# Kernel optimization log

Measured on AMD Instinct MI355X. Metric: run time of the kernel, lower is better.

## Reference

```python
import jax, jax.numpy as jnp
import numpy as np
import math

B, S, H, NH = 2, 1024, 768, 12
DH = H // NH  # 64

def setup_inputs() -> dict:
    key = jax.random.key(0)
    ks = jax.random.split(key, 8)
    sc = 0.02
    return {
        "hidden_states": jax.random.normal(ks[0], (B, S, H), jnp.float32),
        "bbox_pos_emb": jax.random.normal(ks[1], (S, S, B, DH), jnp.float32),
        "attention_mask": jnp.zeros((B, 1, 1, S), jnp.float32),
        "Wq": jax.random.normal(ks[2], (H, H), jnp.float32) * sc,
        "bq": jnp.zeros((H,), jnp.float32),
        "Wk": jax.random.normal(ks[3], (H, H), jnp.float32) * sc,
        "bk": jnp.zeros((H,), jnp.float32),
        "Wv": jax.random.normal(ks[4], (H, H), jnp.float32) * sc,
        "bv": jnp.zeros((H,), jnp.float32),
    }

def reference(hidden_states, bbox_pos_emb, attention_mask, Wq, bq, Wk, bk, Wv, bv):
    b, s, h = hidden_states.shape
    def proj(W, bias):
        # (b, s, h) -> (b, nh, s, dh)
        y = hidden_states @ W.T + bias
        return y.reshape(b, s, NH, DH).transpose(0, 2, 1, 3)
    q = proj(Wq, bq)
    k = proj(Wk, bk)
    v = proj(Wv, bv)
    # QK^T: (b, nh, s, s)
    scores = jnp.einsum("bnid,bnjd->bnij", q, k)
    # bbox bias: (s, s, b, dh) -> (b, s, s, dh); bnid,bijd->bnij
    bbox = bbox_pos_emb.transpose(2, 0, 1, 3)
    scores = scores + jnp.einsum("bnid,bijd->bnij", q, bbox)
    scores = scores / math.sqrt(DH)
    scores = scores + attention_mask
    probs = jax.nn.softmax(scores, axis=-1)
    ctx = jnp.einsum("bnij,bnjd->bnid", probs, v)
    ctx = ctx.transpose(0, 2, 1, 3).reshape(b, s, h)
    return ctx
```

## Files before the change

kernel.cpp:

```cpp
#include <hip/hip_runtime.h>
#include <hip/hip_bf16.h>

typedef short bf4 __attribute__((ext_vector_type(4)));
typedef short short8 __attribute__((ext_vector_type(8)));
typedef float f32x4 __attribute__((ext_vector_type(4)));

#define MFMA(a, b, c) __builtin_amdgcn_mfma_f32_16x16x32_bf16((a), (b), (c), 0, 0, 0)

#define NB 2
#define NS 1024
#define NHID 768
#define NHEAD 12
#define NDH 64

__device__ __forceinline__ short f2bf(float x) {
    __hip_bfloat16 h = __float2bfloat16(x);
    return *reinterpret_cast<short*>(&h);
}

__device__ __forceinline__ int xcd_swz(int orig, int nwg) {
    return (orig & 7) * (nwg >> 3) + (orig >> 3);
}

typedef const __attribute__((address_space(1))) void gas_t;
typedef __attribute__((address_space(3))) void las_t;
__device__ __forceinline__ void gld_lds16(const float* g, float* l) {
    __builtin_amdgcn_global_load_lds((gas_t*)g, (las_t*)l, 16, 0, 0);
}
__device__ __forceinline__ void gld_lds16s(const short* g, short* l) {
    __builtin_amdgcn_global_load_lds((gas_t*)g, (las_t*)l, 16, 0, 0);
}

#define NHE (2048 * 768)
#define WE  (768 * 768)
__global__ void cvt_bf16_all(
    const float* __restrict__ hidden,
    const float* __restrict__ Wq, const float* __restrict__ Wk,
    const float* __restrict__ Wv,
    short* __restrict__ Xbf, short* __restrict__ Wbf)
{
    const int base = (blockIdx.x * 256 + threadIdx.x) * 4;
    const float* src; short* dst; int off;
    if (base < NHE)               { src = hidden; dst = Xbf;          off = base; }
    else if (base < NHE + WE)     { src = Wq;     dst = Wbf;          off = base - NHE; }
    else if (base < NHE + 2 * WE) { src = Wk;     dst = Wbf + WE;     off = base - NHE - WE; }
    else                          { src = Wv;     dst = Wbf + 2 * WE; off = base - NHE - 2 * WE; }
    f32x4 v = *reinterpret_cast<const f32x4*>(src + off);
    bf4 r;
    r[0] = f2bf(v[0]); r[1] = f2bf(v[1]); r[2] = f2bf(v[2]); r[3] = f2bf(v[3]);
    *reinterpret_cast<bf4*>(dst + off) = r;
}

__device__ __forceinline__ void qkv_block(
    int m0, int n0,
    const short* __restrict__ Xbf, const short* __restrict__ Wbf,
    const float* __restrict__ bq, const float* __restrict__ bk,
    const float* __restrict__ bv,
    short* __restrict__ Qo, short* __restrict__ Ko, short* __restrict__ VTo,
    short (*Alds)[4096], short (*Blds)[4096])
{
    const int lane = threadIdx.x & 63;
    const int wave = threadIdx.x >> 6;
    const int lg = lane >> 4, lr = lane & 15;

    const int proj = n0 / NHID;
    const int ncol0 = n0 % NHID;
    const float* bias = proj == 0 ? bq : (proj == 1 ? bk : bv);

    f32x4 acc[4];
    #pragma unroll
    for (int s = 0; s < 4; ++s) acc[s] = (f32x4){0.f, 0.f, 0.f, 0.f};

    auto stage = [&](int t, int buf) {
        const int k0 = t * 64;
        #pragma unroll
        for (int p = 0; p < 2; ++p) {
            const int op = wave * 2 + p;
            const int unit = op * 64 + lane;
            const int r = unit >> 3, u = unit & 7;
            const int g = u ^ (r & 7);
            gld_lds16s(Xbf + (size_t)(m0 + r) * NHID + k0 + g * 8,
                       &Alds[buf][op * 512]);
        }
        #pragma unroll
        for (int p = 0; p < 2; ++p) {
            const int op = wave * 2 + p;
            const int unit = op * 64 + lane;
            const int r = unit >> 3, u = unit & 7;
            const int g = u ^ (r & 7);
            gld_lds16s(Wbf + (size_t)(n0 + r) * NHID + k0 + g * 8,
                       &Blds[buf][op * 512]);
        }
    };

    auto compute = [&](int buf) {
        #pragma unroll
        for (int kk = 0; kk < 2; ++kk) {
            const int U = kk * 4 + lg;
            const int Ra = wave * 16 + lr;
            short8 a = *reinterpret_cast<const short8*>(
                &Alds[buf][(Ra * 8 + (U ^ (Ra & 7))) * 8]);
            #pragma unroll
            for (int s = 0; s < 4; ++s) {
                const int R = s * 16 + lr;
                short8 b = *reinterpret_cast<const short8*>(
                    &Blds[buf][(R * 8 + (U ^ (R & 7))) * 8]);
                acc[s] = MFMA(a, b, acc[s]);
            }
        }
    };

    stage(0, 0);
    for (int t = 0; t < 12; ++t) {
        if (t < 11) {
            stage(t + 1, (t + 1) % 3);
            asm volatile("s_waitcnt vmcnt(4)" ::: "memory");
        } else {
            asm volatile("s_waitcnt vmcnt(0)" ::: "memory");
        }
        __builtin_amdgcn_s_barrier();
        compute(t % 3);
    }

    #pragma unroll
    for (int s = 0; s < 4; ++s) {
        const int ncol = ncol0 + s * 16 + lr;
        const float badd = bias[ncol];
        #pragma unroll
        for (int r = 0; r < 4; ++r) {
            const int m = m0 + wave * 16 + lg * 4 + r;
            const short v16 = f2bf(acc[s][r] + badd);
            if (proj == 0) {
                Qo[(size_t)m * NHID + ncol] = v16;
            } else if (proj == 1) {
                Ko[(size_t)m * NHID + ncol] = v16;
            } else {
                const int b = m >> 10, ss = m & 1023;
                const int h = ncol >> 6, dd = ncol & 63;
                VTo[(((size_t)(b * NHEAD + h) * NDH + dd) << 10) + ss] = v16;
            }
        }
    }
}

__device__ __forceinline__ void bias_block(
    int i,
    const short* __restrict__ Q,
    const float* __restrict__ bbox,
    const float* __restrict__ mask,
    short* __restrict__ biasH,
    float (*lds)[2][2048])
{
    const int lane = threadIdx.x & 63;
    const int wave = threadIdx.x >> 6;
    const int lg = lane >> 4, lr = lane & 15;
    const int jq = wave * 256;

    short8 qa[2][2];
    #pragma unroll
    for (int b2 = 0; b2 < 2; ++b2)
        #pragma unroll
        for (int kk = 0; kk < 2; ++kk)
            qa[b2][kk] = *reinterpret_cast<const short8*>(
                Q + ((size_t)(b2 * NS) + i) * NHID + lr * 64 + kk * 32 + lg * 8);

    const int r_half = lane >> 5;
    const int u_lin = lane & 31;

    auto stage = [&](int t, int buf) {
        const int j0 = jq + t * 16;
        float* dst = &lds[wave][buf][0];
        #pragma unroll
        for (int w = 0; w < 8; ++w) {
            const int r = 2 * w + r_half;
            const int u = u_lin ^ (r & 7);
            const float* src = bbox + (size_t)(i * NS + j0 + r) * 128 + u * 4;
            gld_lds16(src, dst + w * 256);
        }
    };

    auto compute = [&](int t, int buf) {
        const float* tile = &lds[wave][buf][0];
        const int j0 = jq + t * 16;
        const int x = lr & 7;
        #pragma unroll
        for (int b2 = 0; b2 < 2; ++b2) {
            const float mk = mask[b2 * NS + j0 + lr];
            f32x4 c = (f32x4){0.f, 0.f, 0.f, 0.f};
            #pragma unroll
            for (int kk = 0; kk < 2; ++kk) {
                const int q0 = b2 * 16 + kk * 8 + lg * 2;
                f32x4 ca = *reinterpret_cast<const f32x4*>(tile + (size_t)(lr * 32 + ((q0)     ^ x)) * 4);
                f32x4 cb = *reinterpret_cast<const f32x4*>(tile + (size_t)(lr * 32 + ((q0 + 1) ^ x)) * 4);
                short8 bf;
                bf[0] = f2bf(ca[0]); bf[1] = f2bf(ca[1]); bf[2] = f2bf(ca[2]); bf[3] = f2bf(ca[3]);
                bf[4] = f2bf(cb[0]); bf[5] = f2bf(cb[1]); bf[6] = f2bf(cb[2]); bf[7] = f2bf(cb[3]);
                c = MFMA(qa[b2][kk], bf, c);
            }
            if (lg < 3) {
                #pragma unroll
                for (int r = 0; r < 4; ++r) {
                    const int n = lg * 4 + r;
                    biasH[((size_t)(b2 * NHEAD + n) * NS + i) * NS + j0 + lr] =
                        f2bf(c[r] * 0.125f + mk);
                }
            }
        }
    };

    stage(0, 0);
    for (int t = 0; t < 16; ++t) {
        const int buf = t & 1;
        asm volatile("s_waitcnt lgkmcnt(0)" ::: "memory");
        if (t < 15) stage(t + 1, buf ^ 1);
        if (t == 0 || t == 15) asm volatile("s_waitcnt vmcnt(8)"  ::: "memory");
        else                   asm volatile("s_waitcnt vmcnt(16)" ::: "memory");
        compute(t, buf);
    }
}

__global__ __launch_bounds__(256, 3) void q_gemm(
    const short* __restrict__ Xbf, const short* __restrict__ Wbf,
    const float* __restrict__ bq, const float* __restrict__ bk,
    const float* __restrict__ bv,
    short* __restrict__ Qo, short* __restrict__ Ko, short* __restrict__ VTo)
{
    __shared__ short Alds[3][4096];
    __shared__ short Blds[3][4096];
    const int s = xcd_swz(blockIdx.x, 384);
    const int m0 = (s / 12) * 64;
    const int n0 = (s % 12) * 64;
    qkv_block(m0, n0, Xbf, Wbf, bq, bk, bv, Qo, Ko, VTo, Alds, Blds);
}

__global__ __launch_bounds__(256, 2) void bias_kv(
    const short* __restrict__ Qw,
    const float* __restrict__ bbox,
    const float* __restrict__ mask,
    short* __restrict__ biasH,
    const short* __restrict__ Xbf, const short* __restrict__ Wbf,
    const float* __restrict__ bq, const float* __restrict__ bk,
    const float* __restrict__ bv,
    short* __restrict__ Ko, short* __restrict__ VTo)
{
    __shared__ __align__(16) char smem[65536];
    const int bid = blockIdx.x;
    const int grp = bid / 7, rem = bid % 7;
    if (rem < 4) {
        const int i = grp * 4 + rem;
        bias_block(i, Qw, bbox, mask, biasH, (float(*)[2][2048])smem);
    } else {
        const int kvid = grp * 3 + (rem - 4);
        const int s = xcd_swz(kvid, 768);
        const int m0 = (s / 24) * 64;
        const int n0 = NHID + (s % 24) * 64;
        qkv_block(m0, n0, Xbf, Wbf, bq, bk, bv,
                  nullptr, Ko, VTo,
                  (short(*)[4096])smem, (short(*)[4096])(smem + 24576));
    }
}

__global__ __launch_bounds__(256, 3) void attn3(
    const short* __restrict__ Q,
    const short* __restrict__ K,
    const short* __restrict__ VT,
    const short* __restrict__ biasH,
    float* __restrict__ out)
{
    const int tid = threadIdx.x;
    const int lane = tid & 63;
    const int wave = tid >> 6;
    const int lg = lane >> 4, lr = lane & 15;

    const int wgid = xcd_swz(blockIdx.x, 24 * 16);
    const int bh = wgid >> 4;
    const int ic = wgid & 15;
    const int b = bh / NHEAD, h = bh % NHEAD;
    const int i0 = ic * 64 + wave * 16;

    __shared__ short Klds[3][2048];
    __shared__ short Vlds[3][2048];
    __shared__ short Blds[3][2048];
    __shared__ short plds[4][16 * 40];

    short8 qa[2];
    #pragma unroll
    for (int kk = 0; kk < 2; ++kk)
        qa[kk] = *reinterpret_cast<const short8*>(
            Q + ((size_t)(b * NS) + i0 + lr) * NHID + h * 64 + kk * 32 + lg * 8);

    const short* Kb = K + (size_t)b * NS * NHID + h * 64;
    const short* Vb = VT + (size_t)(b * NHEAD + h) * NDH * NS;
    const short* Bb = biasH + ((size_t)(b * NHEAD + h) * NS + ic * 64) * NS;

    f32x4 ctx[4];
    #pragma unroll
    for (int dt = 0; dt < 4; ++dt) ctx[dt] = (f32x4){0.f, 0.f, 0.f, 0.f};
    f32x4 den = (f32x4){0.f, 0.f, 0.f, 0.f};

    const int kr = tid >> 3, ku = tid & 7;
    const int kgu = ku ^ (kr & 7);
    const int vr = tid >> 2, vu = tid & 3;
    const int vgu = vu ^ (vr & 3);
    const int br = tid >> 2, bu = tid & 3;

    auto stage = [&](int t, int buf) {
        const int j0 = t * 32;
        gld_lds16s(Kb + (size_t)(j0 + kr) * NHID + kgu * 8, &Klds[buf][tid * 8]);
        gld_lds16s(Vb + (size_t)vr * NS + j0 + vgu * 8,     &Vlds[buf][tid * 8]);
        gld_lds16s(Bb + (size_t)br * NS + j0 + bu * 8,      &Blds[buf][tid * 8]);
    };

    auto compute = [&](int buf) {
        f32x4 sc[2];
        #pragma unroll
        for (int s = 0; s < 2; ++s) {
            f32x4 c = (f32x4){0.f, 0.f, 0.f, 0.f};
            #pragma unroll
            for (int kk = 0; kk < 2; ++kk) {
                const int R = s * 16 + lr;
                const int U = kk * 4 + lg;
                short8 kf = *reinterpret_cast<const short8*>(
                    &Klds[buf][(R * 8 + (U ^ (R & 7))) * 8]);
                c = MFMA(qa[kk], kf, c);
            }
            sc[s] = c;
        }
        #pragma unroll
        for (int s = 0; s < 2; ++s)
            #pragma unroll
            for (int r = 0; r < 4; ++r) {
                const unsigned int u = (unsigned int)(unsigned short)
                    Blds[buf][wave * 512 + (lg * 4 + r) * 32 + s * 16 + lr] << 16;
                float bb;
                __builtin_memcpy(&bb, &u, 4);
                sc[s][r] = __expf(sc[s][r] * 0.125f + bb);
            }
        den += sc[0] + sc[1];

        #pragma unroll
        for (int s = 0; s < 2; ++s)
            #pragma unroll
            for (int r = 0; r < 4; ++r)
                plds[wave][(lg * 4 + r) * 40 + s * 16 + lr] = f2bf(sc[s][r]);
        asm volatile("" ::: "memory");
        short8 pa = *reinterpret_cast<const short8*>(&plds[wave][lr * 40 + lg * 8]);
        asm volatile("" ::: "memory");

        #pragma unroll
        for (int dt = 0; dt < 4; ++dt) {
            const int R = dt * 16 + lr;
            short8 vf = *reinterpret_cast<const short8*>(
                &Vlds[buf][(R * 4 + (lg ^ (R & 3))) * 8]);
            ctx[dt] = MFMA(pa, vf, ctx[dt]);
        }
    };

    stage(0, 0);
    for (int t = 0; t < 32; ++t) {
        if (t < 31) {
            stage(t + 1, (t + 1) % 3);
            asm volatile("s_waitcnt vmcnt(3)" ::: "memory");
        } else {
            asm volatile("s_waitcnt vmcnt(0)" ::: "memory");
        }
        __builtin_amdgcn_s_barrier();
        compute(t % 3);
    }

    #pragma unroll
    for (int w = 1; w < 16; w <<= 1) {
        f32x4 o;
        #pragma unroll
        for (int r = 0; r < 4; ++r) o[r] = __shfl_xor(den[r], w, 64);
        den += o;
    }

    #pragma unroll
    for (int r = 0; r < 4; ++r) {
        const float inv = 1.0f / den[r];
        const int i = i0 + lg * 4 + r;
        #pragma unroll
        for (int dt = 0; dt < 4; ++dt)
            out[((size_t)(b * NS) + i) * NHID + h * 64 + dt * 16 + lr] =
                ctx[dt][r] * inv;
    }
}

extern "C" void kernel_launch(void* const* d_in, const int* in_sizes, int n_in,
                              void* d_out, int out_size, void* d_ws, size_t ws_size,
                              hipStream_t stream) {
    (void)in_sizes; (void)n_in; (void)out_size; (void)ws_size;
    const float* hidden = (const float*)d_in[0];
    const float* bbox   = (const float*)d_in[1];
    const float* mask   = (const float*)d_in[2];
    const float* Wq = (const float*)d_in[3]; const float* bq = (const float*)d_in[4];
    const float* Wk = (const float*)d_in[5]; const float* bk = (const float*)d_in[6];
    const float* Wv = (const float*)d_in[7]; const float* bv = (const float*)d_in[8];
    float* out = (float*)d_out;

    char* ws = (char*)d_ws;
    const size_t qkv_bytes = (size_t)NB * NS * NHID * sizeof(short);
    short* Qw  = (short*)ws;
    short* Kw  = (short*)(ws + qkv_bytes);
    short* VTw = (short*)(ws + 2 * qkv_bytes);
    short* biasH = (short*)(ws + 3 * qkv_bytes);
    const size_t bias_bytes = (size_t)NB * NHEAD * NS * NS * sizeof(short);
    short* Xbf = (short*)(ws + 3 * qkv_bytes + bias_bytes);
    short* Wbf = Xbf + (size_t)2048 * NHID;

    const int cvt_total = (NHE + 3 * WE) / 4;
    cvt_bf16_all<<<cvt_total / 256, 256, 0, stream>>>(hidden, Wq, Wk, Wv, Xbf, Wbf);

    q_gemm<<<384, 256, 0, stream>>>(Xbf, Wbf, bq, bk, bv, Qw, Kw, VTw);

    bias_kv<<<1792, 256, 0, stream>>>(Qw, bbox, mask, biasH,
                                      Xbf, Wbf, bq, bk, bv, Kw, VTw);

    attn3<<<24 * 16, 256, 0, stream>>>(Qw, Kw, VTw, biasH, out);
}
```

Baseline: 191.5 us.

## Fuse fp32-to-bf16 conversion into QKV GEMM staging and halve attention block size

Removes the separate conversion kernel. The QKV GEMM now stages fp32 hidden and weight tiles into LDS and converts them to bf16 in registers just before each MFMA. This uses K-tiles of 32 instead of 64, so the loop runs twice as many iterations. The attention kernel is also split into blocks of two waves covering 32 query rows each, doubling the grid to 768 blocks for better CU occupancy. The trade-offs are extra conversion ALU work, more global bytes per GEMM tile (fp32), more barriers, and re-reading K/V tiles across twice as many blocks.

```diff
diff --git a/kernel.cpp b/kernel.cpp
--- a/kernel.cpp
+++ b/kernel.cpp
@@ -31,33 +31,15 @@
     __builtin_amdgcn_global_load_lds((gas_t*)g, (las_t*)l, 16, 0, 0);
 }
 
-#define NHE (2048 * 768)
-#define WE  (768 * 768)
-__global__ void cvt_bf16_all(
+__device__ __forceinline__ void qkv_block_f32(
+    int m0, int n0,
     const float* __restrict__ hidden,
     const float* __restrict__ Wq, const float* __restrict__ Wk,
     const float* __restrict__ Wv,
-    short* __restrict__ Xbf, short* __restrict__ Wbf)
-{
-    const int base = (blockIdx.x * 256 + threadIdx.x) * 4;
-    const float* src; short* dst; int off;
-    if (base < NHE)               { src = hidden; dst = Xbf;          off = base; }
-    else if (base < NHE + WE)     { src = Wq;     dst = Wbf;          off = base - NHE; }
-    else if (base < NHE + 2 * WE) { src = Wk;     dst = Wbf + WE;     off = base - NHE - WE; }
-    else                          { src = Wv;     dst = Wbf + 2 * WE; off = base - NHE - 2 * WE; }
-    f32x4 v = *reinterpret_cast<const f32x4*>(src + off);
-    bf4 r;
-    r[0] = f2bf(v[0]); r[1] = f2bf(v[1]); r[2] = f2bf(v[2]); r[3] = f2bf(v[3]);
-    *reinterpret_cast<bf4*>(dst + off) = r;
-}
-
-__device__ __forceinline__ void qkv_block(
-    int m0, int n0,
-    const short* __restrict__ Xbf, const short* __restrict__ Wbf,
     const float* __restrict__ bq, const float* __restrict__ bk,
     const float* __restrict__ bv,
     short* __restrict__ Qo, short* __restrict__ Ko, short* __restrict__ VTo,
-    short (*Alds)[4096], short (*Blds)[4096])
+    float (*Alds)[2048], float (*Blds)[2048])
 {
     const int lane = threadIdx.x & 63;
     const int wave = threadIdx.x >> 6;
@@ -65,6 +47,7 @@
 
     const int proj = n0 / NHID;
     const int ncol0 = n0 % NHID;
+    const float* W = proj == 0 ? Wq : (proj == 1 ? Wk : Wv);
     const float* bias = proj == 0 ? bq : (proj == 1 ? bk : bv);
 
     f32x4 acc[4];
@@ -72,47 +55,51 @@
     for (int s = 0; s < 4; ++s) acc[s] = (f32x4){0.f, 0.f, 0.f, 0.f};
 
     auto stage = [&](int t, int buf) {
-        const int k0 = t * 64;
+        const int k0 = t * 32;
         #pragma unroll
         for (int p = 0; p < 2; ++p) {
-            const int op = wave * 2 + p;
-            const int unit = op * 64 + lane;
+            const int unit = (wave * 2 + p) * 64 + lane;
             const int r = unit >> 3, u = unit & 7;
             const int g = u ^ (r & 7);
-            gld_lds16s(Xbf + (size_t)(m0 + r) * NHID + k0 + g * 8,
-                       &Alds[buf][op * 512]);
+            gld_lds16(hidden + (size_t)(m0 + r) * NHID + k0 + g * 4,
+                      &Alds[buf][unit * 4]);
         }
         #pragma unroll
         for (int p = 0; p < 2; ++p) {
-            const int op = wave * 2 + p;
-            const int unit = op * 64 + lane;
+            const int unit = (wave * 2 + p) * 64 + lane;
             const int r = unit >> 3, u = unit & 7;
             const int g = u ^ (r & 7);
-            gld_lds16s(Wbf + (size_t)(n0 + r) * NHID + k0 + g * 8,
-                       &Blds[buf][op * 512]);
+            gld_lds16(W + (size_t)(ncol0 + r) * NHID + k0 + g * 4,
+                      &Blds[buf][unit * 4]);
         }
     };
 
     auto compute = [&](int buf) {
-        #pragma unroll
-        for (int kk = 0; kk < 2; ++kk) {
-            const int U = kk * 4 + lg;
-            const int Ra = wave * 16 + lr;
-            short8 a = *reinterpret_cast<const short8*>(
-                &Alds[buf][(Ra * 8 + (U ^ (Ra & 7))) * 8]);
-            #pragma unroll
-            for (int s = 0; s < 4; ++s) {
-                const int R = s * 16 + lr;
-                short8 b = *reinterpret_cast<const short8*>(
-                    &Blds[buf][(R * 8 + (U ^ (R & 7))) * 8]);
-                acc[s] = MFMA(a, b, acc[s]);
-            }
+        const int Ra = wave * 16 + lr;
+        f32x4 a0 = *reinterpret_cast<const f32x4*>(
+            &Alds[buf][(Ra * 8 + ((2 * lg)     ^ (Ra & 7))) * 4]);
+        f32x4 a1 = *reinterpret_cast<const f32x4*>(
+            &Alds[buf][(Ra * 8 + ((2 * lg + 1) ^ (Ra & 7))) * 4]);
+        short8 af;
+        af[0] = f2bf(a0[0]); af[1] = f2bf(a0[1]); af[2] = f2bf(a0[2]); af[3] = f2bf(a0[3]);
+        af[4] = f2bf(a1[0]); af[5] = f2bf(a1[1]); af[6] = f2bf(a1[2]); af[7] = f2bf(a1[3]);
+        #pragma unroll
+        for (int s = 0; s < 4; ++s) {
+            const int R = s * 16 + lr;
+            f32x4 b0 = *reinterpret_cast<const f32x4*>(
+                &Blds[buf][(R * 8 + ((2 * lg)     ^ (R & 7))) * 4]);
+            f32x4 b1 = *reinterpret_cast<const f32x4*>(
+                &Blds[buf][(R * 8 + ((2 * lg + 1) ^ (R & 7))) * 4]);
+            short8 bf;
+            bf[0] = f2bf(b0[0]); bf[1] = f2bf(b0[1]); bf[2] = f2bf(b0[2]); bf[3] = f2bf(b0[3]);
+            bf[4] = f2bf(b1[0]); bf[5] = f2bf(b1[1]); bf[6] = f2bf(b1[2]); bf[7] = f2bf(b1[3]);
+            acc[s] = MFMA(af, bf, acc[s]);
         }
     };
 
     stage(0, 0);
-    for (int t = 0; t < 12; ++t) {
-        if (t < 11) {
+    for (int t = 0; t < 24; ++t) {
+        if (t < 23) {
             stage(t + 1, (t + 1) % 3);
             asm volatile("s_waitcnt vmcnt(4)" ::: "memory");
         } else {
@@ -220,17 +207,20 @@
 }
 
 __global__ __launch_bounds__(256, 3) void q_gemm(
-    const short* __restrict__ Xbf, const short* __restrict__ Wbf,
+    const float* __restrict__ hidden,
+    const float* __restrict__ Wq, const float* __restrict__ Wk,
+    const float* __restrict__ Wv,
     const float* __restrict__ bq, const float* __restrict__ bk,
     const float* __restrict__ bv,
     short* __restrict__ Qo, short* __restrict__ Ko, short* __restrict__ VTo)
 {
-    __shared__ short Alds[3][4096];
-    __shared__ short Blds[3][4096];
+    __shared__ float Alds[3][2048];
+    __shared__ float Blds[3][2048];
     const int s = xcd_swz(blockIdx.x, 384);
     const int m0 = (s / 12) * 64;
     const int n0 = (s % 12) * 64;
-    qkv_block(m0, n0, Xbf, Wbf, bq, bk, bv, Qo, Ko, VTo, Alds, Blds);
+    qkv_block_f32(m0, n0, hidden, Wq, Wk, Wv, bq, bk, bv,
+                  Qo, Ko, VTo, Alds, Blds);
 }
 
 __global__ __launch_bounds__(256, 2) void bias_kv(
@@ -238,7 +228,9 @@
     const float* __restrict__ bbox,
     const float* __restrict__ mask,
     short* __restrict__ biasH,
-    const short* __restrict__ Xbf, const short* __restrict__ Wbf,
+    const float* __restrict__ hidden,
+    const float* __restrict__ Wq, const float* __restrict__ Wk,
+    const float* __restrict__ Wv,
     const float* __restrict__ bq, const float* __restrict__ bk,
     const float* __restrict__ bv,
     short* __restrict__ Ko, short* __restrict__ VTo)
@@ -254,13 +246,13 @@
         const int s = xcd_swz(kvid, 768);
         const int m0 = (s / 24) * 64;
         const int n0 = NHID + (s % 24) * 64;
-        qkv_block(m0, n0, Xbf, Wbf, bq, bk, bv,
-                  nullptr, Ko, VTo,
-                  (short(*)[4096])smem, (short(*)[4096])(smem + 24576));
-    }
-}
-
-__global__ __launch_bounds__(256, 3) void attn3(
+        qkv_block_f32(m0, n0, hidden, Wq, Wk, Wv, bq, bk, bv,
+                      nullptr, Ko, VTo,
+                      (float(*)[2048])smem, (float(*)[2048])(smem + 24576));
+    }
+}
+
+__global__ __launch_bounds__(128, 2) void attn3(
     const short* __restrict__ Q,
     const short* __restrict__ K,
     const short* __restrict__ VT,
@@ -272,16 +264,16 @@
     const int wave = tid >> 6;
     const int lg = lane >> 4, lr = lane & 15;
 
-    const int wgid = xcd_swz(blockIdx.x, 24 * 16);
-    const int bh = wgid >> 4;
-    const int ic = wgid & 15;
+    const int wgid = xcd_swz(blockIdx.x, 24 * 32);
+    const int bh = wgid >> 5;
+    const int ic = wgid & 31;
     const int b = bh / NHEAD, h = bh % NHEAD;
-    const int i0 = ic * 64 + wave * 16;
+    const int i0 = ic * 32 + wave * 16;
 
     __shared__ short Klds[3][2048];
     __shared__ short Vlds[3][2048];
-    __shared__ short Blds[3][2048];
-    __shared__ short plds[4][16 * 40];
+    __shared__ short Blds[3][1024];
+    __shared__ short plds[2][16 * 40];
 
     short8 qa[2];
     #pragma unroll
@@ -291,24 +283,33 @@
 
     const short* Kb = K + (size_t)b * NS * NHID + h * 64;
     const short* Vb = VT + (size_t)(b * NHEAD + h) * NDH * NS;
-    const short* Bb = biasH + ((size_t)(b * NHEAD + h) * NS + ic * 64) * NS;
+    const short* Bb = biasH + ((size_t)(b * NHEAD + h) * NS + ic * 32) * NS;
 
     f32x4 ctx[4];
     #pragma unroll
     for (int dt = 0; dt < 4; ++dt) ctx[dt] = (f32x4){0.f, 0.f, 0.f, 0.f};
     f32x4 den = (f32x4){0.f, 0.f, 0.f, 0.f};
 
-    const int kr = tid >> 3, ku = tid & 7;
-    const int kgu = ku ^ (kr & 7);
-    const int vr = tid >> 2, vu = tid & 3;
-    const int vgu = vu ^ (vr & 3);
-    const int br = tid >> 2, bu = tid & 3;
-
     auto stage = [&](int t, int buf) {
         const int j0 = t * 32;
-        gld_lds16s(Kb + (size_t)(j0 + kr) * NHID + kgu * 8, &Klds[buf][tid * 8]);
-        gld_lds16s(Vb + (size_t)vr * NS + j0 + vgu * 8,     &Vlds[buf][tid * 8]);
-        gld_lds16s(Bb + (size_t)br * NS + j0 + bu * 8,      &Blds[buf][tid * 8]);
+        #pragma unroll
+        for (int p = 0; p < 2; ++p) {
+            const int unit = p * 128 + tid;
+            const int r = unit >> 3, u = unit & 7;
+            const int g = u ^ (r & 7);
+            gld_lds16s(Kb + (size_t)(j0 + r) * NHID + g * 8, &Klds[buf][unit * 8]);
+        }
+        #pragma unroll
+        for (int p = 0; p < 2; ++p) {
+            const int unit = p * 128 + tid;
+            const int r = unit >> 2, u = unit & 3;
+            const int g = u ^ (r & 3);
+            gld_lds16s(Vb + (size_t)r * NS + j0 + g * 8, &Vlds[buf][unit * 8]);
+        }
+        {
+            const int r = tid >> 2, u = tid & 3;
+            gld_lds16s(Bb + (size_t)r * NS + j0 + u * 8, &Blds[buf][tid * 8]);
+        }
     };
 
     auto compute = [&](int buf) {
@@ -331,7 +332,7 @@
             #pragma unroll
             for (int r = 0; r < 4; ++r) {
                 const unsigned int u = (unsigned int)(unsigned short)
-                    Blds[buf][wave * 512 + (lg * 4 + r) * 32 + s * 16 + lr] << 16;
+                    Blds[buf][(wave * 16 + lg * 4 + r) * 32 + s * 16 + lr] << 16;
                 float bb;
                 __builtin_memcpy(&bb, &u, 4);
                 sc[s][r] = __expf(sc[s][r] * 0.125f + bb);
@@ -360,7 +361,7 @@
     for (int t = 0; t < 32; ++t) {
         if (t < 31) {
             stage(t + 1, (t + 1) % 3);
-            asm volatile("s_waitcnt vmcnt(3)" ::: "memory");
+            asm volatile("s_waitcnt vmcnt(5)" ::: "memory");
         } else {
             asm volatile("s_waitcnt vmcnt(0)" ::: "memory");
         }
@@ -405,17 +406,13 @@
     short* Kw  = (short*)(ws + qkv_bytes);
     short* VTw = (short*)(ws + 2 * qkv_bytes);
     short* biasH = (short*)(ws + 3 * qkv_bytes);
-    const size_t bias_bytes = (size_t)NB * NHEAD * NS * NS * sizeof(short);
-    short* Xbf = (short*)(ws + 3 * qkv_bytes + bias_bytes);
-    short* Wbf = Xbf + (size_t)2048 * NHID;
-
-    const int cvt_total = (NHE + 3 * WE) / 4;
-    cvt_bf16_all<<<cvt_total / 256, 256, 0, stream>>>(hidden, Wq, Wk, Wv, Xbf, Wbf);
-
-    q_gemm<<<384, 256, 0, stream>>>(Xbf, Wbf, bq, bk, bv, Qw, Kw, VTw);
+
+    q_gemm<<<384, 256, 0, stream>>>(hidden, Wq, Wk, Wv, bq, bk, bv,
+                                    Qw, Kw, VTw);
 
     bias_kv<<<1792, 256, 0, stream>>>(Qw, bbox, mask, biasH,
-                                      Xbf, Wbf, bq, bk, bv, Kw, VTw);
-
-    attn3<<<24 * 16, 256, 0, stream>>>(Qw, Kw, VTw, biasH, out);
-}
+                                      hidden, Wq, Wk, Wv, bq, bk, bv,
+                                      Kw, VTw);
+
+    attn3<<<24 * 32, 128, 0, stream>>>(Qw, Kw, VTw, biasH, out);
+}
```

Result: slower. 201.0 us (+5.0%).
